# Kernel optimization log

Measured on AMD Instinct MI355X. Metric: run time of the kernel, lower is better.

Reference implementation:

```python
import jax, jax.numpy as jnp
import numpy as np

B, C, F, T = 4, 64, 256, 256
CH = C // 2  # self.n_ch inside the module
EPS = 1e-5


def _cbp(x, W, b, g, be, m, v, a):
    # 1x1 conv == channel matmul, then BatchNorm (inference stats) + PReLU (scalar slope)
    y = jnp.einsum('oi,bift->boft', W, x) + b[None, :, None, None]
    y = (y - m[None, :, None, None]) * jax.lax.rsqrt(v[None, :, None, None] + EPS)
    y = y * g[None, :, None, None] + be[None, :, None, None]
    return jnp.where(y > 0, y, a * y)


def setup_inputs() -> dict:
    key = jax.random.key(0)
    ks = jax.random.split(key, 16)

    def conv_params(i, cin, cout, pre):
        W = jax.random.normal(ks[i], (cout, cin), dtype=jnp.float32) * 0.05
        return {
            pre + '_W': W,
            pre + '_b': jnp.zeros((cout,), jnp.float32),
            pre + '_g': jnp.ones((cout,), jnp.float32),
            pre + '_be': jnp.zeros((cout,), jnp.float32),
            pre + '_m': jax.random.normal(ks[i + 1], (cout,), dtype=jnp.float32) * 0.1,
            pre + '_v': jax.random.uniform(ks[i + 2], (cout,), dtype=jnp.float32) + 0.5,
            pre + '_a': jnp.float32(0.25),
        }

    d = {
        'inp': jax.random.normal(ks[12], (B, C, F, T), dtype=jnp.float32),
        'x': jax.random.normal(ks[13], (B, C, F, T), dtype=jnp.float32),
    }
    d.update(conv_params(0, C, 2 * CH, 'fqk'))
    d.update(conv_params(3, C, CH, 'fv'))
    d.update(conv_params(6, C, 2 * CH, 'tqk'))
    d.update(conv_params(9, CH, C, 'proj'))
    return d


def reference(inp, x,
              fqk_W, fqk_b, fqk_g, fqk_be, fqk_m, fqk_v, fqk_a,
              fv_W, fv_b, fv_g, fv_be, fv_m, fv_v, fv_a,
              tqk_W, tqk_b, tqk_g, tqk_be, tqk_m, tqk_v, tqk_a,
              proj_W, proj_b, proj_g, proj_be, proj_m, proj_v, proj_a):
    scale = 1.0 / jnp.sqrt(jnp.float32(CH))

    # frequency attention
    f_qk = _cbp(inp, fqk_W, fqk_b, fqk_g, fqk_be, fqk_m, fqk_v, fqk_a)  # B,2CH,F,T
    vf = _cbp(x, fv_W, fv_b, fv_g, fv_be, fv_m, fv_v, fv_a)             # B,CH,F,T
    r = f_qk.reshape(f_qk.shape[0], CH, 2, F, T)  # 'b (c k) f t -> b c k f t'
    qf, kf = r[:, :, 0], r[:, :, 1]
    f_score = jnp.einsum('bcft,bcyt->btfy', qf, kf) * scale
    f_score = jax.nn.softmax(f_score, axis=-1)
    fout = jnp.einsum('btfy,bcyt->bcft', f_score, vf)

    # time attention (causal mask)
    t_qk = _cbp(inp, tqk_W, tqk_b, tqk_g, tqk_be, tqk_m, tqk_v, tqk_a)
    r = t_qk.reshape(t_qk.shape[0], CH, 2, F, T)
    qt, kt = r[:, :, 0], r[:, :, 1]
    t_score = jnp.einsum('bcft,bcfy->bfty', qt, kt) * scale
    mask = jnp.triu(jnp.ones((T, T), dtype=bool), k=1)  # j - i + 1 with i == j
    neg = -jnp.finfo(t_score.dtype).max
    t_score = jnp.where(mask, neg, t_score)
    t_score = jax.nn.softmax(t_score, axis=-1)
    tout = jnp.einsum('bfty,bcfy->bcft', t_score, fout)

    out = _cbp(tout, proj_W, proj_b, proj_g, proj_be, proj_m, proj_v, proj_a)
    return out + x
```

## Files before the change

### kernel.cpp

```cpp
#include <hip/hip_runtime.h>
#include <hip/hip_bf16.h>

typedef __hip_bfloat16 bf16;
typedef __attribute__((ext_vector_type(8))) short bf16x8;
typedef __attribute__((ext_vector_type(4))) float f32x4;
typedef __attribute__((ext_vector_type(16))) float f32x16;
typedef __attribute__((ext_vector_type(8))) unsigned short u16x8;
typedef __attribute__((ext_vector_type(4))) unsigned int u32x4;
typedef __attribute__((ext_vector_type(2))) unsigned int u32x2;

struct ConvP {
  const float* W; const float* bi; const float* g; const float* be;
  const float* m; const float* v; const float* a;
};

#define QS (0.17677669529663687f * 1.4426950408889634f)

__device__ __forceinline__ int swz1024(int i) {
  return ((i & 7) << 7) | (i >> 3);
}

__device__ __forceinline__ unsigned short f2bf(float f) {
  __hip_bfloat16 h = __float2bfloat16(f);
  return __builtin_bit_cast(unsigned short, h);
}
__device__ __forceinline__ float fast_exp2(float x) {
#if __has_builtin(__builtin_amdgcn_exp2f)
  return __builtin_amdgcn_exp2f(x);
#else
  return exp2f(x);
#endif
}

__global__ __launch_bounds__(256, 2) void conv_qkv(
    const float* __restrict__ inp, const float* __restrict__ x,
    ConvP fqk, ConvP fv, ConvP tqk,
    bf16* __restrict__ Qf, bf16* __restrict__ Kf, bf16* __restrict__ Vf,
    bf16* __restrict__ Qt, bf16* __restrict__ Kt)
{
  __shared__ __attribute__((aligned(16))) unsigned short Xb[64 * 260];
  __shared__ __attribute__((aligned(16))) unsigned short S0[256 * 40];
  __shared__ __attribute__((aligned(16))) unsigned short S1[256 * 40];
  __shared__ __attribute__((aligned(8)))  float2 Pc[160];

  const int tid = threadIdx.x;
  const int b = blockIdx.x >> 8;
  const int f = blockIdx.x & 255;
  const size_t gbase = (size_t)b * 64 * 65536 + f * 256;
  const size_t tbase = (size_t)(b * 256 + f) * 8192;

  const int lane = tid & 63;
  const int wid = tid >> 6;
  const int m16 = lane & 15;
  const int quad = lane >> 4;

  if (tid < 160) {
    const ConvP& P = (tid < 64) ? fqk : (tid < 128) ? tqk : fv;
    const int o = (tid < 64) ? tid : (tid < 128) ? tid - 64 : tid - 128;
    float A = P.g[o] * rsqrtf(P.v[o] + 1e-5f);
    float B2 = (P.bi[o] - P.m[o]) * A + P.be[o];
    if (tid < 128 && ((o & 1) == 0)) { A *= QS; B2 *= QS; }
    Pc[tid] = make_float2(A, B2);
  }

  auto load_X = [&](const float* __restrict__ src) {
    #pragma unroll
    for (int r = 0; r < 16; ++r) {
      const int idx = r * 256 + tid;
      const int c = idx >> 6;
      const int t0 = (idx & 63) * 4;
      const float4 v = *(const float4*)(src + gbase + (size_t)c * 65536 + t0);
      unsigned lo = (unsigned)f2bf(v.x) | (((unsigned)f2bf(v.y)) << 16);
      unsigned hi = (unsigned)f2bf(v.z) | (((unsigned)f2bf(v.w)) << 16);
      u32x2 pk = {lo, hi};
      *(u32x2*)&Xb[c * 260 + t0] = pk;
    }
  };

  auto load_A = [&](const float* __restrict__ W, int rowbase, int ks) {
    const float* p = W + (rowbase + m16) * 64 + ks * 32 + quad * 8;
    const float4 lo = *(const float4*)p;
    const float4 hi = *(const float4*)(p + 4);
    bf16x8 r;
    r[0] = (short)f2bf(lo.x); r[1] = (short)f2bf(lo.y);
    r[2] = (short)f2bf(lo.z); r[3] = (short)f2bf(lo.w);
    r[4] = (short)f2bf(hi.x); r[5] = (short)f2bf(hi.y);
    r[6] = (short)f2bf(hi.z); r[7] = (short)f2bf(hi.w);
    return r;
  };

  auto load_B = [&](int tt, int ks) {
    const int t = tt * 16 + m16;
    const int i0 = ks * 32 + quad * 8;
    bf16x8 r;
    #pragma unroll
    for (int j = 0; j < 8; ++j) r[j] = (short)Xb[(i0 + j) * 260 + t];
    return r;
  };

  auto emit = [&](const unsigned short* S, bf16* __restrict__ dst) {
    #pragma unroll
    for (int r = 0; r < 4; ++r) {
      const int chunk = r * 256 + tid;
      const int t = chunk >> 2, part = chunk & 3;
      u32x4 v = *(const u32x4*)&S[t * 40 + part * 8];
      *(u32x4*)(dst + tbase + (size_t)chunk * 8) = v;
    }
  };

  auto leaky = [](float y, float alpha) { return y > 0.f ? y : alpha * y; };

  auto qk_pass = [&](const ConvP& P, int pcb, const bf16x8 (&Bf)[4][2]) {
    bf16x8 A[4][2];
    #pragma unroll
    for (int ot = 0; ot < 4; ++ot)
      #pragma unroll
      for (int ks = 0; ks < 2; ++ks) A[ot][ks] = load_A(P.W, ot * 16, ks);
    float pA[4][4], pB[4][4];
    #pragma unroll
    for (int ot = 0; ot < 4; ++ot)
      #pragma unroll
      for (int r = 0; r < 4; ++r) {
        const float2 pp = Pc[pcb + ot * 16 + quad * 4 + r];
        pA[ot][r] = pp.x; pB[ot][r] = pp.y;
      }
    const float alpha = P.a[0];
    #pragma unroll
    for (int i = 0; i < 4; ++i) {
      const int t = (wid * 4 + i) * 16 + m16;
      #pragma unroll
      for (int ot = 0; ot < 4; ++ot) {
        f32x4 acc = {0.f, 0.f, 0.f, 0.f};
        acc = __builtin_amdgcn_mfma_f32_16x16x32_bf16(A[ot][0], Bf[i][0], acc, 0, 0, 0);
        acc = __builtin_amdgcn_mfma_f32_16x16x32_bf16(A[ot][1], Bf[i][1], acc, 0, 0, 0);
        float y[4];
        #pragma unroll
        for (int r = 0; r < 4; ++r)
          y[r] = leaky(acc[r] * pA[ot][r] + pB[ot][r], alpha);
        const int ch0 = ot * 8 + quad * 2;
        *(unsigned*)&S0[t * 40 + ch0] = (unsigned)f2bf(y[0]) | (((unsigned)f2bf(y[2])) << 16);
        *(unsigned*)&S1[t * 40 + ch0] = (unsigned)f2bf(y[1]) | (((unsigned)f2bf(y[3])) << 16);
      }
    }
  };

  load_X(inp);
  __syncthreads();

  bf16x8 Bf[4][2];
  #pragma unroll
  for (int i = 0; i < 4; ++i)
    #pragma unroll
    for (int ks = 0; ks < 2; ++ks) Bf[i][ks] = load_B(wid * 4 + i, ks);

  qk_pass(fqk, 0, Bf);
  __syncthreads();
  emit(S0, Qf); emit(S1, Kf);
  __syncthreads();
  qk_pass(tqk, 64, Bf);
  __syncthreads();
  emit(S0, Qt); emit(S1, Kt);
  __syncthreads();
  load_X(x);
  __syncthreads();

  {
    bf16x8 A[2][2], Bv[4][2];
    #pragma unroll
    for (int i = 0; i < 4; ++i)
      #pragma unroll
      for (int ks = 0; ks < 2; ++ks) Bv[i][ks] = load_B(wid * 4 + i, ks);
    #pragma unroll
    for (int ot = 0; ot < 2; ++ot)
      #pragma unroll
      for (int ks = 0; ks < 2; ++ks) A[ot][ks] = load_A(fv.W, ot * 16, ks);
    float pA[2][4], pB[2][4];
    #pragma unroll
    for (int ot = 0; ot < 2; ++ot)
      #pragma unroll
      for (int r = 0; r < 4; ++r) {
        const float2 pp = Pc[128 + ot * 16 + quad * 4 + r];
        pA[ot][r] = pp.x; pB[ot][r] = pp.y;
      }
    const float alpha = fv.a[0];
    #pragma unroll
    for (int i = 0; i < 4; ++i) {
      const int t = (wid * 4 + i) * 16 + m16;
      #pragma unroll
      for (int ot = 0; ot < 2; ++ot) {
        f32x4 acc = {0.f, 0.f, 0.f, 0.f};
        acc = __builtin_amdgcn_mfma_f32_16x16x32_bf16(A[ot][0], Bv[i][0], acc, 0, 0, 0);
        acc = __builtin_amdgcn_mfma_f32_16x16x32_bf16(A[ot][1], Bv[i][1], acc, 0, 0, 0);
        float y[4];
        #pragma unroll
        for (int r = 0; r < 4; ++r)
          y[r] = leaky(acc[r] * pA[ot][r] + pB[ot][r], alpha);
        const int ch = ot * 16 + quad * 4;
        *(unsigned*)&S0[t * 40 + ch]     = (unsigned)f2bf(y[0]) | (((unsigned)f2bf(y[1])) << 16);
        *(unsigned*)&S0[t * 40 + ch + 2] = (unsigned)f2bf(y[2]) | (((unsigned)f2bf(y[3])) << 16);
      }
    }
  }
  __syncthreads();
  emit(S0, Vf);
}

template<bool CAUSAL>
__global__ __launch_bounds__(256, 2) void attn_k(
    const bf16* __restrict__ Qg, const bf16* __restrict__ Kg,
    const bf16* __restrict__ Vg, bf16* __restrict__ Og)
{
  __shared__ __attribute__((aligned(16))) unsigned short Kl[256 * 40];
  __shared__ __attribute__((aligned(16))) unsigned short Vt[32 * 264];
  __shared__ __attribute__((aligned(16))) unsigned short Plds[4][16 * 264];
  __shared__ __attribute__((aligned(16))) unsigned short Wsc[4][16 * 40];

  const int inst = swz1024(blockIdx.x);
  const int b = inst >> 8;
  const int s = inst & 255;
  constexpr int RS = CAUSAL ? 32 : 8192;
  const int qbase = CAUSAL ? inst * 8192 : (b * 2097152 + s * 32);

  const int tid = threadIdx.x;
  const int lane = tid & 63;
  const int wid = tid >> 6;
  const int m16 = lane & 15;
  const int quad = lane >> 4;
  const int r4 = lane >> 2, p4 = lane & 3;

  u32x4 qpre[4];
  #pragma unroll
  for (int it = 0; it < 4; ++it) {
    const int rt = wid + 4 * it;
    qpre[it] = *(const u32x4*)(Qg + qbase + (rt * 16 + r4) * RS + p4 * 8);
  }

  #pragma unroll
  for (int k2 = 0; k2 < 4; ++k2) {
    const int chunk = k2 * 256 + tid;
    const int row = chunk >> 2, part = chunk & 3;
    u32x4 val = *(const u32x4*)(Kg + qbase + row * RS + part * 8);
    *(u32x4*)&Kl[row * 40 + part * 8] = val;
  }
  if (tid < 128) {
    const unsigned short* v0 = (const unsigned short*)(Vg + qbase) + (2 * tid) * RS;
    const unsigned short* v1 = v0 + RS;
    u16x8 a[4], c[4];
    #pragma unroll
    for (int q = 0; q < 4; ++q) {
      a[q] = *(const u16x8*)(v0 + 8 * q);
      c[q] = *(const u16x8*)(v1 + 8 * q);
    }
    unsigned int* vt32 = (unsigned int*)Vt;
    #pragma unroll
    for (int cc = 0; cc < 32; ++cc) {
      unsigned lo = a[cc >> 3][cc & 7];
      unsigned hi = c[cc >> 3][cc & 7];
      vt32[(cc * 264 + 2 * tid) >> 1] = lo | (hi << 16);
    }
  }
  __syncthreads();

  unsigned short* P  = &Plds[wid][0];
  unsigned short* Ws = &Wsc[wid][0];

  bf16x8 kfr[16];
  #pragma unroll
  for (int ct = 0; ct < 16; ++ct)
    kfr[ct] = *(const bf16x8*)&Kl[(ct * 16 + m16) * 40 + quad * 8];

  #pragma unroll 1
  for (int it = 0; it < 4; ++it) {
    const int rt = wid + 4 * it;
    {
      *(u32x4*)&Ws[r4 * 40 + p4 * 8] = qpre[it];
    }
    const bf16x8 qf = *(const bf16x8*)&Ws[m16 * 40 + quad * 8];
    const int nct = CAUSAL ? (rt + 1) : 16;

    f32x4 acc[16];
    #pragma unroll
    for (int ct = 0; ct < 16; ++ct) {
      if (ct < nct) {
        f32x4 z = {0.f, 0.f, 0.f, 0.f};
        acc[ct] = __builtin_amdgcn_mfma_f32_16x16x32_bf16(kfr[ct], qf, z, 0, 0, 0);
      }
    }
    float mxr[4] = {-3e38f, -3e38f, -3e38f, -3e38f};
    #pragma unroll
    for (int ct = 0; ct < 16; ++ct) if (ct < nct) {
      #pragma unroll
      for (int r = 0; r < 4; ++r) {
        float v = acc[ct][r];
        if (CAUSAL && (ct == nct - 1) && (quad * 4 + r > m16)) v = -3e38f;
        acc[ct][r] = v;
        mxr[r] = fmaxf(mxr[r], v);
      }
    }
    float m = fmaxf(fmaxf(mxr[0], mxr[1]), fmaxf(mxr[2], mxr[3]));
    m = fmaxf(m, __shfl_xor(m, 16, 64));
    m = fmaxf(m, __shfl_xor(m, 32, 64));
    float sr[4] = {0.f, 0.f, 0.f, 0.f};
    #pragma unroll
    for (int ct = 0; ct < 16; ++ct) if (ct < nct) {
      #pragma unroll
      for (int r = 0; r < 4; ++r) {
        float p = fast_exp2(acc[ct][r] - m);
        acc[ct][r] = p;
        sr[r] += p;
      }
    }
    float ssum = (sr[0] + sr[1]) + (sr[2] + sr[3]);
    ssum += __shfl_xor(ssum, 16, 64);
    ssum += __shfl_xor(ssum, 32, 64);
    const float inv = 1.0f / ssum;

    #pragma unroll
    for (int ct = 0; ct < 16; ++ct) if (ct < nct) {
      u32x2 pk = { (unsigned)f2bf(acc[ct][0]) | (((unsigned)f2bf(acc[ct][1])) << 16),
                   (unsigned)f2bf(acc[ct][2]) | (((unsigned)f2bf(acc[ct][3])) << 16) };
      *(u32x2*)&P[m16 * 264 + ct * 16 + quad * 4] = pk;
    }
    int ksteps = CAUSAL ? ((rt >> 1) + 1) : 8;
    if (CAUSAL && ((rt & 1) == 0)) {
      u32x2 z2 = {0u, 0u};
      *(u32x2*)&P[m16 * 264 + (rt + 1) * 16 + quad * 4] = z2;
    }
    f32x4 o0 = {0.f, 0.f, 0.f, 0.f}, o1 = {0.f, 0.f, 0.f, 0.f};
    #pragma unroll
    for (int ks = 0; ks < 8; ++ks) {
      if (ks < ksteps) {
        const bf16x8 pf  = *(const bf16x8*)&P[m16 * 264 + ks * 32 + quad * 8];
        const bf16x8 vf0 = *(const bf16x8*)&Vt[m16 * 264 + ks * 32 + quad * 8];
        const bf16x8 vf1 = *(const bf16x8*)&Vt[(16 + m16) * 264 + ks * 32 + quad * 8];
        o0 = __builtin_amdgcn_mfma_f32_16x16x32_bf16(pf, vf0, o0, 0, 0, 0);
        o1 = __builtin_amdgcn_mfma_f32_16x16x32_bf16(pf, vf1, o1, 0, 0, 0);
      }
    }
    #pragma unroll
    for (int r = 0; r < 4; ++r) {
      const float invq = __shfl(inv, quad * 4 + r, 16);
      Ws[(quad * 4 + r) * 40 + m16]      = f2bf(o0[r] * invq);
      Ws[(quad * 4 + r) * 40 + 16 + m16] = f2bf(o1[r] * invq);
    }
    {
      u32x4 ov = *(const u32x4*)&Ws[r4 * 40 + p4 * 8];
      *(u32x4*)(Og + qbase + (rt * 16 + r4) * RS + p4 * 8) = ov;
    }
  }
}

__global__ __launch_bounds__(256) void proj_k(
    const bf16* __restrict__ tout, const float* __restrict__ x,
    ConvP pj, float* __restrict__ out)
{
  __shared__ float2 Pc[64];
  const int tid = threadIdx.x;
  const int id = swz1024(blockIdx.x);
  const int b = id >> 8;
  const int f = id & 255;
  if (tid < 64) {
    const float A = pj.g[tid] * rsqrtf(pj.v[tid] + 1e-5f);
    const float B2 = (pj.bi[tid] - pj.m[tid]) * A + pj.be[tid];
    Pc[tid] = make_float2(A, B2);
  }
  const int lane = tid & 63;
  const int wid = tid >> 6;
  const int n32 = lane & 31;
  const int h = lane >> 5;

  bf16x8 Afr[2][2];
  #pragma unroll
  for (int ot = 0; ot < 2; ++ot)
    #pragma unroll
    for (int ks = 0; ks < 2; ++ks) {
      const float* p = pj.W + (ot * 32 + n32) * 32 + ks * 16 + h * 8;
      const float4 lo = *(const float4*)p;
      const float4 hi = *(const float4*)(p + 4);
      bf16x8 r;
      r[0] = (short)f2bf(lo.x); r[1] = (short)f2bf(lo.y);
      r[2] = (short)f2bf(lo.z); r[3] = (short)f2bf(lo.w);
      r[4] = (short)f2bf(hi.x); r[5] = (short)f2bf(hi.y);
      r[6] = (short)f2bf(hi.z); r[7] = (short)f2bf(hi.w);
      Afr[ot][ks] = r;
    }
  __syncthreads();

  const float alpha = pj.a[0];
  const size_t gbase = (size_t)b * 64 * 65536 + f * 256;
  const size_t tbase = (size_t)(b * 256 + f) * 8192;

  #pragma unroll
  for (int tt = 0; tt < 2; ++tt) {
    const int t = wid * 64 + tt * 32 + n32;
    const bf16x8 B0 = *(const bf16x8*)(tout + tbase + (size_t)t * 32 + 0 * 16 + h * 8);
    const bf16x8 B1 = *(const bf16x8*)(tout + tbase + (size_t)t * 32 + 1 * 16 + h * 8);
    #pragma unroll
    for (int ot = 0; ot < 2; ++ot) {
      f32x16 acc = {};
      acc = __builtin_amdgcn_mfma_f32_32x32x16_bf16(Afr[ot][0], B0, acc, 0, 0, 0);
      acc = __builtin_amdgcn_mfma_f32_32x32x16_bf16(Afr[ot][1], B1, acc, 0, 0, 0);
      #pragma unroll
      for (int reg = 0; reg < 16; ++reg) {
        const int o = ot * 32 + (reg & 3) + 8 * (reg >> 2) + 4 * h;
        const float2 pp = Pc[o];
        float y = acc[reg] * pp.x + pp.y;
        y = y > 0.f ? y : alpha * y;
        const size_t off = gbase + (size_t)o * 65536 + t;
        out[off] = y + x[off];
      }
    }
  }
}

extern "C" void kernel_launch(void* const* d_in, const int* in_sizes, int n_in,
                              void* d_out, int out_size, void* d_ws, size_t ws_size,
                              hipStream_t stream) {
  const float* inp = (const float*)d_in[0];
  const float* x   = (const float*)d_in[1];
  auto cp = [&](int i) {
    return ConvP{ (const float*)d_in[i],     (const float*)d_in[i + 1],
                  (const float*)d_in[i + 2], (const float*)d_in[i + 3],
                  (const float*)d_in[i + 4], (const float*)d_in[i + 5],
                  (const float*)d_in[i + 6] };
  };
  ConvP fqk = cp(2), fv = cp(9), tqk = cp(16), pj = cp(23);

  char* ws = (char*)d_ws;
  const size_t SZ = (size_t)4 * 256 * 256 * 32 * 2;
  bf16* Qf = (bf16*)(ws + 0 * SZ);
  bf16* Kf = (bf16*)(ws + 1 * SZ);
  bf16* Vf = (bf16*)(ws + 2 * SZ);
  bf16* Qt = (bf16*)(ws + 3 * SZ);
  bf16* Kt = (bf16*)(ws + 4 * SZ);
  bf16* Ft = (bf16*)(ws + 5 * SZ);
  bf16* To = (bf16*)(ws + 0 * SZ);

  conv_qkv<<<1024, 256, 0, stream>>>(inp, x, fqk, fv, tqk, Qf, Kf, Vf, Qt, Kt);
  attn_k<false><<<1024, 256, 0, stream>>>(Qf, Kf, Vf, Ft);
  attn_k<true><<<1024, 256, 0, stream>>>(Qt, Kt, Ft, To);
  proj_k<<<1024, 256, 0, stream>>>(To, x, pj, (float*)d_out);
}
```

Measured before the change: 316.5 us.

## Stage conv outputs per wave and prefetch x during QK passes

Replaces the block-wide shared staging buffers and their barrier-separated emit phases with small per-wave staging tiles. Each wave writes its 16-row results and immediately streams them to global memory. The loads of x are split into two register-prefetched halves issued before each QK pass, so global latency overlaps with the MFMA work. Smaller LDS use allows the launch bound to rise to 3 blocks per CU, at the cost of more registers held for the prefetch buffers.

```diff
diff --git a/kernel.cpp b/kernel.cpp
--- a/kernel.cpp
+++ b/kernel.cpp
@@ -32,15 +32,14 @@
 #endif
 }
 
-__global__ __launch_bounds__(256, 2) void conv_qkv(
+__global__ __launch_bounds__(256, 3) void conv_qkv(
     const float* __restrict__ inp, const float* __restrict__ x,
     ConvP fqk, ConvP fv, ConvP tqk,
     bf16* __restrict__ Qf, bf16* __restrict__ Kf, bf16* __restrict__ Vf,
     bf16* __restrict__ Qt, bf16* __restrict__ Kt)
 {
   __shared__ __attribute__((aligned(16))) unsigned short Xb[64 * 260];
-  __shared__ __attribute__((aligned(16))) unsigned short S0[256 * 40];
-  __shared__ __attribute__((aligned(16))) unsigned short S1[256 * 40];
+  __shared__ __attribute__((aligned(16))) unsigned short Sst[4][2][16 * 40];
   __shared__ __attribute__((aligned(8)))  float2 Pc[160];
 
   const int tid = threadIdx.x;
@@ -53,6 +52,10 @@
   const int wid = tid >> 6;
   const int m16 = lane & 15;
   const int quad = lane >> 4;
+  const int r4 = lane >> 2, p4 = lane & 3;
+
+  unsigned short* S0w = &Sst[wid][0][0];
+  unsigned short* S1w = &Sst[wid][1][0];
 
   if (tid < 160) {
     const ConvP& P = (tid < 64) ? fqk : (tid < 128) ? tqk : fv;
@@ -63,19 +66,19 @@
     Pc[tid] = make_float2(A, B2);
   }
 
-  auto load_X = [&](const float* __restrict__ src) {
+  {
     #pragma unroll
     for (int r = 0; r < 16; ++r) {
       const int idx = r * 256 + tid;
       const int c = idx >> 6;
       const int t0 = (idx & 63) * 4;
-      const float4 v = *(const float4*)(src + gbase + (size_t)c * 65536 + t0);
+      const float4 v = *(const float4*)(inp + gbase + (size_t)c * 65536 + t0);
       unsigned lo = (unsigned)f2bf(v.x) | (((unsigned)f2bf(v.y)) << 16);
       unsigned hi = (unsigned)f2bf(v.z) | (((unsigned)f2bf(v.w)) << 16);
       u32x2 pk = {lo, hi};
       *(u32x2*)&Xb[c * 260 + t0] = pk;
     }
-  };
+  }
 
   auto load_A = [&](const float* __restrict__ W, int rowbase, int ks) {
     const float* p = W + (rowbase + m16) * 64 + ks * 32 + quad * 8;
@@ -98,19 +101,10 @@
     return r;
   };
 
-  auto emit = [&](const unsigned short* S, bf16* __restrict__ dst) {
-    #pragma unroll
-    for (int r = 0; r < 4; ++r) {
-      const int chunk = r * 256 + tid;
-      const int t = chunk >> 2, part = chunk & 3;
-      u32x4 v = *(const u32x4*)&S[t * 40 + part * 8];
-      *(u32x4*)(dst + tbase + (size_t)chunk * 8) = v;
-    }
-  };
-
   auto leaky = [](float y, float alpha) { return y > 0.f ? y : alpha * y; };
 
-  auto qk_pass = [&](const ConvP& P, int pcb, const bf16x8 (&Bf)[4][2]) {
+  auto qk_pass = [&](const ConvP& P, int pcb, const bf16x8 (&Bf)[4][2],
+                     bf16* __restrict__ Qd, bf16* __restrict__ Kd) {
     bf16x8 A[4][2];
     #pragma unroll
     for (int ot = 0; ot < 4; ++ot)
@@ -127,7 +121,6 @@
     const float alpha = P.a[0];
     #pragma unroll
     for (int i = 0; i < 4; ++i) {
-      const int t = (wid * 4 + i) * 16 + m16;
       #pragma unroll
       for (int ot = 0; ot < 4; ++ot) {
         f32x4 acc = {0.f, 0.f, 0.f, 0.f};
@@ -138,13 +131,17 @@
         for (int r = 0; r < 4; ++r)
           y[r] = leaky(acc[r] * pA[ot][r] + pB[ot][r], alpha);
         const int ch0 = ot * 8 + quad * 2;
-        *(unsigned*)&S0[t * 40 + ch0] = (unsigned)f2bf(y[0]) | (((unsigned)f2bf(y[2])) << 16);
-        *(unsigned*)&S1[t * 40 + ch0] = (unsigned)f2bf(y[1]) | (((unsigned)f2bf(y[3])) << 16);
-      }
+        *(unsigned*)&S0w[m16 * 40 + ch0] = (unsigned)f2bf(y[0]) | (((unsigned)f2bf(y[2])) << 16);
+        *(unsigned*)&S1w[m16 * 40 + ch0] = (unsigned)f2bf(y[1]) | (((unsigned)f2bf(y[3])) << 16);
+      }
+      const int trow = (wid * 4 + i) * 16 + r4;
+      u32x4 qv = *(const u32x4*)&S0w[r4 * 40 + p4 * 8];
+      u32x4 kv = *(const u32x4*)&S1w[r4 * 40 + p4 * 8];
+      *(u32x4*)(Qd + tbase + (size_t)trow * 32 + p4 * 8) = qv;
+      *(u32x4*)(Kd + tbase + (size_t)trow * 32 + p4 * 8) = kv;
     }
   };
 
-  load_X(inp);
   __syncthreads();
 
   bf16x8 Bf[4][2];
@@ -153,15 +150,49 @@
     #pragma unroll
     for (int ks = 0; ks < 2; ++ks) Bf[i][ks] = load_B(wid * 4 + i, ks);
 
-  qk_pass(fqk, 0, Bf);
   __syncthreads();
-  emit(S0, Qf); emit(S1, Kf);
-  __syncthreads();
-  qk_pass(tqk, 64, Bf);
-  __syncthreads();
-  emit(S0, Qt); emit(S1, Kt);
-  __syncthreads();
-  load_X(x);
+
+  float4 xpre[8];
+  #pragma unroll
+  for (int r = 0; r < 8; ++r) {
+    const int idx = r * 256 + tid;
+    const int c = idx >> 6;
+    const int t0 = (idx & 63) * 4;
+    xpre[r] = *(const float4*)(x + gbase + (size_t)c * 65536 + t0);
+  }
+
+  qk_pass(fqk, 0, Bf, Qf, Kf);
+
+  #pragma unroll
+  for (int r = 0; r < 8; ++r) {
+    const int idx = r * 256 + tid;
+    const int c = idx >> 6;
+    const int t0 = (idx & 63) * 4;
+    unsigned lo = (unsigned)f2bf(xpre[r].x) | (((unsigned)f2bf(xpre[r].y)) << 16);
+    unsigned hi = (unsigned)f2bf(xpre[r].z) | (((unsigned)f2bf(xpre[r].w)) << 16);
+    u32x2 pk = {lo, hi};
+    *(u32x2*)&Xb[c * 260 + t0] = pk;
+  }
+  #pragma unroll
+  for (int r = 0; r < 8; ++r) {
+    const int idx = (r + 8) * 256 + tid;
+    const int c = idx >> 6;
+    const int t0 = (idx & 63) * 4;
+    xpre[r] = *(const float4*)(x + gbase + (size_t)c * 65536 + t0);
+  }
+
+  qk_pass(tqk, 64, Bf, Qt, Kt);
+
+  #pragma unroll
+  for (int r = 0; r < 8; ++r) {
+    const int idx = (r + 8) * 256 + tid;
+    const int c = idx >> 6;
+    const int t0 = (idx & 63) * 4;
+    unsigned lo = (unsigned)f2bf(xpre[r].x) | (((unsigned)f2bf(xpre[r].y)) << 16);
+    unsigned hi = (unsigned)f2bf(xpre[r].z) | (((unsigned)f2bf(xpre[r].w)) << 16);
+    u32x2 pk = {lo, hi};
+    *(u32x2*)&Xb[c * 260 + t0] = pk;
+  }
   __syncthreads();
 
   {
@@ -185,7 +216,6 @@
     const float alpha = fv.a[0];
     #pragma unroll
     for (int i = 0; i < 4; ++i) {
-      const int t = (wid * 4 + i) * 16 + m16;
       #pragma unroll
       for (int ot = 0; ot < 2; ++ot) {
         f32x4 acc = {0.f, 0.f, 0.f, 0.f};
@@ -196,13 +226,14 @@
         for (int r = 0; r < 4; ++r)
           y[r] = leaky(acc[r] * pA[ot][r] + pB[ot][r], alpha);
         const int ch = ot * 16 + quad * 4;
-        *(unsigned*)&S0[t * 40 + ch]     = (unsigned)f2bf(y[0]) | (((unsigned)f2bf(y[1])) << 16);
-        *(unsigned*)&S0[t * 40 + ch + 2] = (unsigned)f2bf(y[2]) | (((unsigned)f2bf(y[3])) << 16);
-      }
-    }
-  }
-  __syncthreads();
-  emit(S0, Vf);
+        *(unsigned*)&S0w[m16 * 40 + ch]     = (unsigned)f2bf(y[0]) | (((unsigned)f2bf(y[1])) << 16);
+        *(unsigned*)&S0w[m16 * 40 + ch + 2] = (unsigned)f2bf(y[2]) | (((unsigned)f2bf(y[3])) << 16);
+      }
+      const int trow = (wid * 4 + i) * 16 + r4;
+      u32x4 vv = *(const u32x4*)&S0w[r4 * 40 + p4 * 8];
+      *(u32x4*)(Vf + tbase + (size_t)trow * 32 + p4 * 8) = vv;
+    }
+  }
 }
 
 template<bool CAUSAL>
```

New measurement: 330.2 us. 4.3% more time.

## Fuse causal time attention with output projection into one kernel

Applied to the files above, without the earlier changes.

Merges the causal time-attention kernel and the projection/BN/PReLU/residual kernel into a single kernel. The attention output for each (b,f) block is kept in LDS as bf16 and consumed directly by the projection MFMAs, so the intermediate tensor never goes to global memory and back, and one launch is removed. The cost is a much larger LDS footprint per block (K, V-transposed, P scratch and an output tile), which may limit occupancy. A launch-bounds hint of two blocks per CU is set.

```diff
diff --git a/kernel.cpp b/kernel.cpp
--- a/kernel.cpp
+++ b/kernel.cpp
@@ -350,64 +350,204 @@
   }
 }
 
-__global__ __launch_bounds__(256) void proj_k(
-    const bf16* __restrict__ tout, const float* __restrict__ x,
-    ConvP pj, float* __restrict__ out)
+__global__ __launch_bounds__(256, 2) void attn_proj(
+    const bf16* __restrict__ Qg, const bf16* __restrict__ Kg,
+    const bf16* __restrict__ Vg, ConvP pj,
+    const float* __restrict__ x, float* __restrict__ out)
 {
-  __shared__ float2 Pc[64];
+  __shared__ __attribute__((aligned(16))) unsigned short Kl[256 * 40];
+  __shared__ __attribute__((aligned(16))) unsigned short Vt[32 * 264];
+  __shared__ __attribute__((aligned(16))) unsigned short Plds[4][16 * 136];
+  __shared__ __attribute__((aligned(16))) unsigned short Wsc[4][16 * 40];
+  __shared__ __attribute__((aligned(16))) unsigned short Ob[256 * 40];
+  __shared__ __attribute__((aligned(8)))  float2 Pc[64];
+
+  const int inst = swz1024(blockIdx.x);
+  const int b = inst >> 8;
+  const int f = inst & 255;
+  const int qbase = inst * 8192;
+
   const int tid = threadIdx.x;
-  const int id = swz1024(blockIdx.x);
-  const int b = id >> 8;
-  const int f = id & 255;
+  const int lane = tid & 63;
+  const int wid = tid >> 6;
+  const int m16 = lane & 15;
+  const int quad = lane >> 4;
+  const int r4 = lane >> 2, p4 = lane & 3;
+
   if (tid < 64) {
     const float A = pj.g[tid] * rsqrtf(pj.v[tid] + 1e-5f);
     const float B2 = (pj.bi[tid] - pj.m[tid]) * A + pj.be[tid];
     Pc[tid] = make_float2(A, B2);
   }
-  const int lane = tid & 63;
-  const int wid = tid >> 6;
-  const int n32 = lane & 31;
-  const int h = lane >> 5;
-
-  bf16x8 Afr[2][2];
-  #pragma unroll
-  for (int ot = 0; ot < 2; ++ot)
-    #pragma unroll
-    for (int ks = 0; ks < 2; ++ks) {
-      const float* p = pj.W + (ot * 32 + n32) * 32 + ks * 16 + h * 8;
-      const float4 lo = *(const float4*)p;
-      const float4 hi = *(const float4*)(p + 4);
-      bf16x8 r;
-      r[0] = (short)f2bf(lo.x); r[1] = (short)f2bf(lo.y);
-      r[2] = (short)f2bf(lo.z); r[3] = (short)f2bf(lo.w);
-      r[4] = (short)f2bf(hi.x); r[5] = (short)f2bf(hi.y);
-      r[6] = (short)f2bf(hi.z); r[7] = (short)f2bf(hi.w);
-      Afr[ot][ks] = r;
-    }
-  __syncthreads();
-
-  const float alpha = pj.a[0];
-  const size_t gbase = (size_t)b * 64 * 65536 + f * 256;
-  const size_t tbase = (size_t)(b * 256 + f) * 8192;
-
-  #pragma unroll
-  for (int tt = 0; tt < 2; ++tt) {
-    const int t = wid * 64 + tt * 32 + n32;
-    const bf16x8 B0 = *(const bf16x8*)(tout + tbase + (size_t)t * 32 + 0 * 16 + h * 8);
-    const bf16x8 B1 = *(const bf16x8*)(tout + tbase + (size_t)t * 32 + 1 * 16 + h * 8);
-    #pragma unroll
-    for (int ot = 0; ot < 2; ++ot) {
-      f32x16 acc = {};
-      acc = __builtin_amdgcn_mfma_f32_32x32x16_bf16(Afr[ot][0], B0, acc, 0, 0, 0);
-      acc = __builtin_amdgcn_mfma_f32_32x32x16_bf16(Afr[ot][1], B1, acc, 0, 0, 0);
-      #pragma unroll
-      for (int reg = 0; reg < 16; ++reg) {
-        const int o = ot * 32 + (reg & 3) + 8 * (reg >> 2) + 4 * h;
-        const float2 pp = Pc[o];
-        float y = acc[reg] * pp.x + pp.y;
-        y = y > 0.f ? y : alpha * y;
-        const size_t off = gbase + (size_t)o * 65536 + t;
-        out[off] = y + x[off];
+
+  u32x4 qpre[4];
+  #pragma unroll
+  for (int it = 0; it < 4; ++it) {
+    const int rt = wid + 4 * it;
+    qpre[it] = *(const u32x4*)(Qg + qbase + (rt * 16 + r4) * 32 + p4 * 8);
+  }
+
+  #pragma unroll
+  for (int k2 = 0; k2 < 4; ++k2) {
+    const int chunk = k2 * 256 + tid;
+    const int row = chunk >> 2, part = chunk & 3;
+    u32x4 val = *(const u32x4*)(Kg + qbase + row * 32 + part * 8);
+    *(u32x4*)&Kl[row * 40 + part * 8] = val;
+  }
+  if (tid < 128) {
+    const unsigned short* v0 = (const unsigned short*)(Vg + qbase) + (2 * tid) * 32;
+    const unsigned short* v1 = v0 + 32;
+    u16x8 a[4], c[4];
+    #pragma unroll
+    for (int q = 0; q < 4; ++q) {
+      a[q] = *(const u16x8*)(v0 + 8 * q);
+      c[q] = *(const u16x8*)(v1 + 8 * q);
+    }
+    unsigned int* vt32 = (unsigned int*)Vt;
+    #pragma unroll
+    for (int cc = 0; cc < 32; ++cc) {
+      unsigned lo = a[cc >> 3][cc & 7];
+      unsigned hi = c[cc >> 3][cc & 7];
+      vt32[(cc * 264 + 2 * tid) >> 1] = lo | (hi << 16);
+    }
+  }
+  __syncthreads();
+
+  unsigned short* P  = &Plds[wid][0];
+  unsigned short* Ws = &Wsc[wid][0];
+
+  bf16x8 kfr[16];
+  #pragma unroll
+  for (int ct = 0; ct < 16; ++ct)
+    kfr[ct] = *(const bf16x8*)&Kl[(ct * 16 + m16) * 40 + quad * 8];
+
+  #pragma unroll 1
+  for (int it = 0; it < 4; ++it) {
+    const int rt = wid + 4 * it;
+    {
+      *(u32x4*)&Ws[r4 * 40 + p4 * 8] = qpre[it];
+    }
+    const bf16x8 qf = *(const bf16x8*)&Ws[m16 * 40 + quad * 8];
+    const int nct = rt + 1;
+
+    f32x4 acc[16];
+    #pragma unroll
+    for (int ct = 0; ct < 16; ++ct) {
+      if (ct < nct) {
+        f32x4 z = {0.f, 0.f, 0.f, 0.f};
+        acc[ct] = __builtin_amdgcn_mfma_f32_16x16x32_bf16(kfr[ct], qf, z, 0, 0, 0);
+      }
+    }
+    float mxr[4] = {-3e38f, -3e38f, -3e38f, -3e38f};
+    #pragma unroll
+    for (int ct = 0; ct < 16; ++ct) if (ct < nct) {
+      #pragma unroll
+      for (int r = 0; r < 4; ++r) {
+        float v = acc[ct][r];
+        if ((ct == nct - 1) && (quad * 4 + r > m16)) v = -3e38f;
+        acc[ct][r] = v;
+        mxr[r] = fmaxf(mxr[r], v);
+      }
+    }
+    float m = fmaxf(fmaxf(mxr[0], mxr[1]), fmaxf(mxr[2], mxr[3]));
+    m = fmaxf(m, __shfl_xor(m, 16, 64));
+    m = fmaxf(m, __shfl_xor(m, 32, 64));
+    float sr[4] = {0.f, 0.f, 0.f, 0.f};
+    #pragma unroll
+    for (int ct = 0; ct < 16; ++ct) if (ct < nct) {
+      #pragma unroll
+      for (int r = 0; r < 4; ++r) {
+        float p = fast_exp2(acc[ct][r] - m);
+        acc[ct][r] = p;
+        sr[r] += p;
+      }
+    }
+    float ssum = (sr[0] + sr[1]) + (sr[2] + sr[3]);
+    ssum += __shfl_xor(ssum, 16, 64);
+    ssum += __shfl_xor(ssum, 32, 64);
+    const float inv = 1.0f / ssum;
+
+    const int ksteps = (rt >> 1) + 1;
+    f32x4 o0 = {0.f, 0.f, 0.f, 0.f}, o1 = {0.f, 0.f, 0.f, 0.f};
+    #pragma unroll
+    for (int hh = 0; hh < 2; ++hh) {
+      if (8 * hh < nct) {
+        #pragma unroll
+        for (int c2 = 0; c2 < 8; ++c2) {
+          const int ct = 8 * hh + c2;
+          if (ct < nct) {
+            u32x2 pk = { (unsigned)f2bf(acc[ct][0]) | (((unsigned)f2bf(acc[ct][1])) << 16),
+                         (unsigned)f2bf(acc[ct][2]) | (((unsigned)f2bf(acc[ct][3])) << 16) };
+            *(u32x2*)&P[m16 * 136 + c2 * 16 + quad * 4] = pk;
+          }
+        }
+        if (((rt & 1) == 0) && (((rt + 1) >> 3) == hh)) {
+          u32x2 z2 = {0u, 0u};
+          *(u32x2*)&P[m16 * 136 + ((rt + 1) & 7) * 16 + quad * 4] = z2;
+        }
+        #pragma unroll
+        for (int k4 = 0; k4 < 4; ++k4) {
+          const int ks = 4 * hh + k4;
+          if (ks < ksteps) {
+            const bf16x8 pf  = *(const bf16x8*)&P[m16 * 136 + k4 * 32 + quad * 8];
+            const bf16x8 vf0 = *(const bf16x8*)&Vt[m16 * 264 + ks * 32 + quad * 8];
+            const bf16x8 vf1 = *(const bf16x8*)&Vt[(16 + m16) * 264 + ks * 32 + quad * 8];
+            o0 = __builtin_amdgcn_mfma_f32_16x16x32_bf16(pf, vf0, o0, 0, 0, 0);
+            o1 = __builtin_amdgcn_mfma_f32_16x16x32_bf16(pf, vf1, o1, 0, 0, 0);
+          }
+        }
+      }
+    }
+    #pragma unroll
+    for (int r = 0; r < 4; ++r) {
+      const float invq = __shfl(inv, quad * 4 + r, 16);
+      const int row = rt * 16 + quad * 4 + r;
+      Ob[row * 40 + m16]      = f2bf(o0[r] * invq);
+      Ob[row * 40 + 16 + m16] = f2bf(o1[r] * invq);
+    }
+  }
+  __syncthreads();
+
+  {
+    const int n32 = lane & 31;
+    const int kh = lane >> 5;
+    bf16x8 Afr[2][2];
+    #pragma unroll
+    for (int ot = 0; ot < 2; ++ot)
+      #pragma unroll
+      for (int ks = 0; ks < 2; ++ks) {
+        const float* p = pj.W + (ot * 32 + n32) * 32 + ks * 16 + kh * 8;
+        const float4 lo = *(const float4*)p;
+        const float4 hi = *(const float4*)(p + 4);
+        bf16x8 r;
+        r[0] = (short)f2bf(lo.x); r[1] = (short)f2bf(lo.y);
+        r[2] = (short)f2bf(lo.z); r[3] = (short)f2bf(lo.w);
+        r[4] = (short)f2bf(hi.x); r[5] = (short)f2bf(hi.y);
+        r[6] = (short)f2bf(hi.z); r[7] = (short)f2bf(hi.w);
+        Afr[ot][ks] = r;
+      }
+    const float alpha = pj.a[0];
+    const size_t gbase = (size_t)b * 64 * 65536 + f * 256;
+
+    #pragma unroll
+    for (int tt = 0; tt < 2; ++tt) {
+      const int t = wid * 64 + tt * 32 + n32;
+      const bf16x8 B0 = *(const bf16x8*)&Ob[t * 40 + 0 * 16 + kh * 8];
+      const bf16x8 B1 = *(const bf16x8*)&Ob[t * 40 + 1 * 16 + kh * 8];
+      #pragma unroll
+      for (int ot = 0; ot < 2; ++ot) {
+        f32x16 acc = {};
+        acc = __builtin_amdgcn_mfma_f32_32x32x16_bf16(Afr[ot][0], B0, acc, 0, 0, 0);
+        acc = __builtin_amdgcn_mfma_f32_32x32x16_bf16(Afr[ot][1], B1, acc, 0, 0, 0);
+        #pragma unroll
+        for (int reg = 0; reg < 16; ++reg) {
+          const int o = ot * 32 + (reg & 3) + 8 * (reg >> 2) + 4 * kh;
+          const float2 pp = Pc[o];
+          float y = acc[reg] * pp.x + pp.y;
+          y = y > 0.f ? y : alpha * y;
+          const size_t off = gbase + (size_t)o * 65536 + t;
+          out[off] = y + x[off];
+        }
       }
     }
   }
@@ -434,10 +574,8 @@
   bf16* Qt = (bf16*)(ws + 3 * SZ);
   bf16* Kt = (bf16*)(ws + 4 * SZ);
   bf16* Ft = (bf16*)(ws + 5 * SZ);
-  bf16* To = (bf16*)(ws + 0 * SZ);
 
   conv_qkv<<<1024, 256, 0, stream>>>(inp, x, fqk, fv, tqk, Qf, Kf, Vf, Qt, Kt);
   attn_k<false><<<1024, 256, 0, stream>>>(Qf, Kf, Vf, Ft);
-  attn_k<true><<<1024, 256, 0, stream>>>(Qt, Kt, Ft, To);
-  proj_k<<<1024, 256, 0, stream>>>(To, x, pj, (float*)d_out);
-}
+  attn_proj<<<1024, 256, 0, stream>>>(Qt, Kt, Ft, pj, x, (float*)d_out);
+}
```

Measured after the change: 309.7 us. 1.02x faster.
